# Kernel optimization log

Hardware: AMD Instinct MI355X
Metric: run time of the kernel (lower is better)

The kernel has to match this reference:

```python
import jax, jax.numpy as jnp
from jax import lax
import numpy as np

DIM, DT_RANK, D_INNER, D_STATE = 256, 16, 256, 16

def _ssm_params(key, d, dt_rank, d_inner, n):
    k1, k2, k3 = jax.random.split(key, 3)
    Wdbc = jax.random.normal(k1, (d, dt_rank + 2 * n), jnp.float32) * 0.02
    Wdt = jax.random.normal(k2, (dt_rank, d_inner), jnp.float32) * 0.02
    bdt = jax.random.normal(k3, (d_inner,), jnp.float32) * 0.02
    Alog = jnp.log(jnp.tile(jnp.arange(1, n + 1, dtype=jnp.float32), (d_inner, 1)))
    D = jnp.ones((d_inner,), jnp.float32)
    return Wdbc, Wdt, bdt, Alog, D

def setup_inputs() -> dict:
    key = jax.random.key(0)
    ks = jax.random.split(key, 10)
    x = jax.random.normal(ks[0], (4, 4096, DIM), jnp.float32)
    ln_g = jnp.ones((DIM,), jnp.float32)
    ln_b = jnp.zeros((DIM,), jnp.float32)
    Wp = jax.random.normal(ks[1], (DIM, DIM), jnp.float32) * 0.02
    bp = jnp.zeros((DIM,), jnp.float32)
    Wcf = jax.random.normal(ks[2], (DIM, DIM), jnp.float32) * 0.02  # conv1d k=1 == pointwise matmul
    bcf = jnp.zeros((DIM,), jnp.float32)
    Wcb = jax.random.normal(ks[3], (DIM, DIM), jnp.float32) * 0.02
    bcb = jnp.zeros((DIM,), jnp.float32)
    Wdbc_f, Wdt_f, bdt_f, Alog_f, D_f = _ssm_params(ks[4], DIM, DT_RANK, D_INNER, D_STATE)
    Wdbc_b, Wdt_b, bdt_b, Alog_b, D_b = _ssm_params(ks[5], DIM, DT_RANK, D_INNER, D_STATE)
    return dict(x=x, ln_g=ln_g, ln_b=ln_b, Wp=Wp, bp=bp, Wcf=Wcf, bcf=bcf, Wcb=Wcb, bcb=bcb,
                Wdbc_f=Wdbc_f, Wdt_f=Wdt_f, bdt_f=bdt_f, Alog_f=Alog_f, D_f=D_f,
                Wdbc_b=Wdbc_b, Wdt_b=Wdt_b, bdt_b=bdt_b, Alog_b=Alog_b, D_b=D_b)

def _layernorm(x, g, b, eps=1e-5):
    mu = jnp.mean(x, -1, keepdims=True)
    var = jnp.var(x, -1, keepdims=True)
    return (x - mu) * lax.rsqrt(var + eps) * g + b

def _selective_scan(x, delta, A, B, C, D):
    # x, delta: [b,s,d]; A: [d,n]; B, C: [b,s,n]; D: [d]
    deltaA = jnp.exp(delta[..., None] * A)              # [b,s,d,n]
    BX = delta[..., None] * B[:, :, None, :] * x[..., None]  # [b,s,d,n]
    dA = jnp.moveaxis(deltaA, 1, 0)
    bx = jnp.moveaxis(BX, 1, 0)
    def step(h, inp):
        dA_t, bx_t = inp
        h = dA_t * h + bx_t
        return h, h
    h0 = jnp.zeros_like(dA[0])
    _, hs = lax.scan(step, h0, (dA, bx))                # [s,b,d,n]
    hs = jnp.moveaxis(hs, 0, 1)                          # [b,s,d,n]
    y = jnp.einsum('bsdn,bsn->bsd', hs, C) + D * x
    return y

def _ssm(x, Wdbc, Wdt, bdt, Alog, D):
    A = -jnp.exp(Alog)
    dbc = x @ Wdbc
    dt_r, B, C = jnp.split(dbc, [DT_RANK, DT_RANK + D_STATE], axis=-1)
    delta = jax.nn.softplus(dt_r @ Wdt + bdt)
    return _selective_scan(x, delta, A, B, C, D)

def _process(x, Wc, bc, Wdbc, Wdt, bdt, Alog, D):
    x = jax.nn.softplus(x @ Wc.T + bc)  # Conv1d k=1: out[e] = sum_d W[e,d] x[d] + b[e]
    return _ssm(x, Wdbc, Wdt, bdt, Alog, D)

def reference(x, ln_g, ln_b, Wp, bp, Wcf, bcf, Wcb, bcb,
              Wdbc_f, Wdt_f, bdt_f, Alog_f, D_f,
              Wdbc_b, Wdt_b, bdt_b, Alog_b, D_b):
    skip = x
    xn = _layernorm(x, ln_g, ln_b)
    z1 = xn @ Wp + bp  # proj used for both z1 and x (same layer twice)
    xp = z1
    x1 = jax.nn.silu(_process(xp, Wcf, bcf, Wdbc_f, Wdt_f, bdt_f, Alog_f, D_f))
    x2r = _process(jnp.flip(xp, 1), Wcb, bcb, Wdbc_b, Wdt_b, bdt_b, Alog_b, D_b)
    x2 = jax.nn.silu(jnp.flip(x2r, 1))
    z = jax.nn.silu(z1)
    return x1 * z + x2 * z + skip
```

## Files before the change

kernel.cpp:

```cpp
#include <hip/hip_runtime.h>
#include <math.h>

#define SB 4
#define SS 4096
#define SD 256
#define SN 16
#define ROWS 16
#define NRB 1024
#define NCH 128
#define CHL 32

#define BM 128
#define BN 64
#define BK 64
#define LDT 72

#define MBM 32
#define MLDZ 264

typedef __attribute__((ext_vector_type(8))) short bf16x8;
typedef __attribute__((ext_vector_type(4))) float f32x4;

__device__ __forceinline__ unsigned short f2bf(float f){
    unsigned int u = __float_as_uint(f);
    u += 0x7FFFu + ((u >> 16) & 1u);
    return (unsigned short)(u >> 16);
}
__device__ __forceinline__ float bf2f(unsigned short u){
    return __uint_as_float(((unsigned int)u) << 16);
}
__device__ __forceinline__ float softplus_f(float x){
    return fmaxf(x, 0.f) + __logf(1.f + __expf(-fabsf(x)));
}
__device__ __forceinline__ float silu_f(float x){
    return x * __builtin_amdgcn_rcpf(1.f + __expf(-x));
}

__global__ __launch_bounds__(256)
void k_prep(const float* __restrict__ Wp,
            const float* __restrict__ Wcf, const float* __restrict__ Wcb,
            const float* __restrict__ Wdbc0, const float* __restrict__ Wdt0,
            const float* __restrict__ Wdbc1, const float* __restrict__ Wdt1,
            unsigned short* __restrict__ WpT, unsigned short* __restrict__ Wc,
            unsigned short* __restrict__ G3W)
{
    int idx = blockIdx.x*256 + threadIdx.x;
    if (idx < 65536){
        int n = idx >> 8, k = idx & 255;
        WpT[idx] = f2bf(Wp[k*256 + n]);
    } else if (idx < 65536 + 131072){
        int j = idx - 65536;
        Wc[j] = f2bf(j < 65536 ? Wcf[j] : Wcb[j - 65536]);
    } else {
        int j = idx - 196608;
        int dir = j / 81920; int r = j - dir*81920;
        int n = r >> 8, d = r & 255;
        const float* Wdbc = dir ? Wdbc1 : Wdbc0;
        const float* Wdt  = dir ? Wdt1  : Wdt0;
        float v;
        if (n < 256){
            v = 0.f;
            #pragma unroll
            for (int q = 0; q < 16; ++q)
                v = fmaf(Wdbc[d*48 + q], Wdt[q*256 + n], v);
        } else if (n < 272) v = Wdbc[d*48 + 16 + (n-256)];
        else if (n < 288)   v = Wdbc[d*48 + 32 + (n-272)];
        else                v = 0.f;
        G3W[(size_t)dir*81920 + r] = f2bf(v);
    }
}

__global__ __launch_bounds__(256)
void k_ln(const float* __restrict__ x, const float* __restrict__ g,
          const float* __restrict__ bln, unsigned short* __restrict__ xnbf){
    int row0 = blockIdx.x * ROWS;
    int tid = threadIdx.x; int w = tid >> 6; int lane = tid & 63;
    #pragma unroll
    for (int rep = 0; rep < 4; ++rep){
        int j = rep*4 + w;
        const float* xr = x + (size_t)(row0 + j)*SD;
        float4 v = *(const float4*)(xr + lane*4);
        float s = v.x + v.y + v.z + v.w;
        #pragma unroll
        for (int off = 32; off; off >>= 1) s += __shfl_xor(s, off, 64);
        float mu = s * (1.f/256.f);
        float d0 = v.x-mu, d1 = v.y-mu, d2 = v.z-mu, d3 = v.w-mu;
        float q = d0*d0 + d1*d1 + d2*d2 + d3*d3;
        #pragma unroll
        for (int off = 32; off; off >>= 1) q += __shfl_xor(q, off, 64);
        float rstd = rsqrtf(q*(1.f/256.f) + 1e-5f);
        float4 gg = *(const float4*)(g + lane*4);
        float4 bb = *(const float4*)(bln + lane*4);
        ushort4 o;
        o.x = f2bf(d0*rstd*gg.x + bb.x);
        o.y = f2bf(d1*rstd*gg.y + bb.y);
        o.z = f2bf(d2*rstd*gg.z + bb.z);
        o.w = f2bf(d3*rstd*gg.w + bb.w);
        *(ushort4*)(xnbf + (size_t)(row0+j)*SD + lane*4) = o;
    }
}

__global__ __launch_bounds__(256, 5)
void k_gemm0(const unsigned short* __restrict__ A,
             const unsigned short* __restrict__ Bt,
             const float* __restrict__ bias0,
             unsigned short* __restrict__ obf)
{
    __shared__ unsigned short sMem[(BM + BN) * LDT];
    unsigned short (*sA)[LDT] = (unsigned short (*)[LDT])sMem;
    unsigned short (*sB)[LDT] = (unsigned short (*)[LDT])(sMem + BM*LDT);
    int ntile = blockIdx.x, mtile = blockIdx.y;
    int row0 = mtile * BM;
    int col0 = ntile * BN;

    int tid = threadIdx.x;
    uint4 ra[4], rb[2];
    auto gload = [&](int kt){
        int k0 = kt * BK;
        #pragma unroll
        for (int i = 0; i < 4; ++i){
            int idx = tid + i*256; int r = idx >> 3, kp = idx & 7;
            ra[i] = *(const uint4*)(A + (size_t)(row0 + r)*256 + k0 + kp*8);
        }
        #pragma unroll
        for (int i = 0; i < 2; ++i){
            int idx = tid + i*256; int r = idx >> 3, kp = idx & 7;
            rb[i] = *(const uint4*)(Bt + (size_t)(col0 + r)*256 + k0 + kp*8);
        }
    };
    auto swrite = [&](){
        #pragma unroll
        for (int i = 0; i < 4; ++i){
            int idx = tid + i*256; int r = idx >> 3, kp = idx & 7;
            *(uint4*)&sA[r][kp*8] = ra[i];
        }
        #pragma unroll
        for (int i = 0; i < 2; ++i){
            int idx = tid + i*256; int r = idx >> 3, kp = idx & 7;
            *(uint4*)&sB[r][kp*8] = rb[i];
        }
    };

    gload(0); swrite(); __syncthreads();

    int lane = tid & 63, w = tid >> 6;
    int wr = w >> 1, wc = w & 1;
    int lr = lane & 15, hi = lane >> 4;

    f32x4 acc[4][2];
    #pragma unroll
    for (int mf = 0; mf < 4; ++mf)
        #pragma unroll
        for (int nf = 0; nf < 2; ++nf)
            acc[mf][nf] = f32x4{0.f, 0.f, 0.f, 0.f};

    for (int kt = 0; kt < 4; ++kt){
        if (kt < 3) gload(kt + 1);
        #pragma unroll
        for (int kk = 0; kk < BK; kk += 32){
            bf16x8 af[4], bfr[2];
            #pragma unroll
            for (int mf = 0; mf < 4; ++mf)
                af[mf] = *(const bf16x8*)&sA[wr*64 + mf*16 + lr][kk + hi*8];
            #pragma unroll
            for (int nf = 0; nf < 2; ++nf)
                bfr[nf] = *(const bf16x8*)&sB[wc*32 + nf*16 + lr][kk + hi*8];
            #pragma unroll
            for (int mf = 0; mf < 4; ++mf)
                #pragma unroll
                for (int nf = 0; nf < 2; ++nf)
                    acc[mf][nf] = __builtin_amdgcn_mfma_f32_16x16x32_bf16(
                        af[mf], bfr[nf], acc[mf][nf], 0, 0, 0);
        }
        if (kt < 3){
            __syncthreads();
            swrite();
            __syncthreads();
        }
    }

    __syncthreads();
    unsigned short (*sOut)[LDT] = (unsigned short (*)[LDT])sMem;
    #pragma unroll
    for (int mf = 0; mf < 4; ++mf){
        #pragma unroll
        for (int nf = 0; nf < 2; ++nf){
            int col = col0 + wc*32 + nf*16 + lr;
            float bias = bias0[col];
            #pragma unroll
            for (int r = 0; r < 4; ++r)
                sOut[wr*64 + mf*16 + hi*4 + r][wc*32 + nf*16 + lr] =
                    f2bf(acc[mf][nf][r] + bias);
        }
    }
    __syncthreads();
    #pragma unroll
    for (int p = 0; p < 4; ++p){
        int chunk = tid + p*256;
        int r = chunk >> 3, cg = chunk & 7;
        uint4 v = *(const uint4*)&sOut[r][cg*8];
        *(uint4*)(obf + (size_t)(row0 + r)*256 + col0 + cg*8) = v;
    }
}

__global__ __launch_bounds__(256, 4)
void k_mid(const unsigned short* __restrict__ z1bf,
           const unsigned short* __restrict__ Wc,
           const unsigned short* __restrict__ G3W,
           const float* __restrict__ bc0, const float* __restrict__ bc1,
           const float* __restrict__ bdt0, const float* __restrict__ bdt1,
           unsigned short* __restrict__ xcbf,
           unsigned short* __restrict__ dg0, unsigned short* __restrict__ dg1,
           float* __restrict__ Bg0, float* __restrict__ Bg1,
           float* __restrict__ Cg0, float* __restrict__ Cg1)
{
    __shared__ unsigned short sZ[MBM*MLDZ];
    __shared__ unsigned short sX[MBM*MLDZ];
    int mtile = blockIdx.x, dir = blockIdx.y;
    int row0 = mtile*MBM;
    int tid = threadIdx.x;
    int lane = tid & 63, w = tid >> 6;
    int lr = lane & 15, hi = lane >> 4;

    {
        const uint4* src = (const uint4*)(z1bf + (size_t)row0*256);
        #pragma unroll
        for (int p = 0; p < 4; ++p){
            int idx = tid + p*256;
            int r = idx >> 5, cq = idx & 31;
            *(uint4*)&sZ[r*MLDZ + cq*8] = src[idx];
        }
    }
    __syncthreads();

    const float* bcp  = dir ? bc1  : bc0;
    const float* bdtp = dir ? bdt1 : bdt0;
    unsigned short* dgp = dir ? dg1 : dg0;
    const unsigned short* Wcp = Wc + (size_t)dir*65536;
    const unsigned short* Gp  = G3W + (size_t)dir*81920;

    f32x4 acc1[4][2];
    #pragma unroll
    for (int nt1 = 0; nt1 < 4; ++nt1)
        #pragma unroll
        for (int mf = 0; mf < 2; ++mf)
            acc1[nt1][mf] = f32x4{0.f,0.f,0.f,0.f};
    #pragma unroll
    for (int kt = 0; kt < 4; ++kt){
        #pragma unroll
        for (int kk2 = 0; kk2 < 2; ++kk2){
            int ko = kt*64 + kk2*32 + hi*8;
            bf16x8 wf[4];
            #pragma unroll
            for (int nt1 = 0; nt1 < 4; ++nt1)
                wf[nt1] = *(const bf16x8*)(Wcp + (size_t)(nt1*64 + w*16 + lr)*256 + ko);
            bf16x8 zf0 = *(const bf16x8*)&sZ[(     lr)*MLDZ + ko];
            bf16x8 zf1 = *(const bf16x8*)&sZ[(16 + lr)*MLDZ + ko];
            #pragma unroll
            for (int nt1 = 0; nt1 < 4; ++nt1){
                acc1[nt1][0] = __builtin_amdgcn_mfma_f32_16x16x32_bf16(wf[nt1], zf0, acc1[nt1][0], 0,0,0);
                acc1[nt1][1] = __builtin_amdgcn_mfma_f32_16x16x32_bf16(wf[nt1], zf1, acc1[nt1][1], 0,0,0);
            }
        }
    }
    #pragma unroll
    for (int nt1 = 0; nt1 < 4; ++nt1){
        #pragma unroll
        for (int mf = 0; mf < 2; ++mf){
            float4 bb = *(const float4*)(bcp + nt1*64 + w*16 + hi*4);
            ushort4 o;
            o.x = f2bf(softplus_f(acc1[nt1][mf][0] + bb.x));
            o.y = f2bf(softplus_f(acc1[nt1][mf][1] + bb.y));
            o.z = f2bf(softplus_f(acc1[nt1][mf][2] + bb.z));
            o.w = f2bf(softplus_f(acc1[nt1][mf][3] + bb.w));
            *(ushort4*)&sX[(mf*16 + lr)*MLDZ + nt1*64 + w*16 + hi*4] = o;
        }
    }
    __syncthreads();
    {
        #pragma unroll
        for (int p = 0; p < 4; ++p){
            int idx = tid + p*256;
            int r = idx >> 5, cq = idx & 31;
            *(uint4*)(xcbf + (size_t)(row0 + r)*512 + dir*256 + cq*8) =
                *(const uint4*)&sX[r*MLDZ + cq*8];
        }
    }

    f32x4 acc2[5][2];
    #pragma unroll
    for (int t5 = 0; t5 < 5; ++t5)
        #pragma unroll
        for (int mf = 0; mf < 2; ++mf)
            acc2[t5][mf] = f32x4{0.f,0.f,0.f,0.f};
    #pragma unroll
    for (int nt1 = 0; nt1 < 4; ++nt1){
        bf16x8 af[2][2];
        #pragma unroll
        for (int mf = 0; mf < 2; ++mf)
            #pragma unroll
            for (int k2 = 0; k2 < 2; ++k2)
                af[mf][k2] = *(const bf16x8*)&sX[(mf*16 + lr)*MLDZ + nt1*64 + k2*32 + hi*8];
        #pragma unroll
        for (int k2 = 0; k2 < 2; ++k2){
            int ko = nt1*64 + k2*32 + hi*8;
            bf16x8 gf[5];
            #pragma unroll
            for (int nt2 = 0; nt2 < 5; ++nt2)
                gf[nt2] = *(const bf16x8*)(Gp + (size_t)(nt2*64 + w*16 + lr)*256 + ko);
            #pragma unroll
            for (int nt2 = 0; nt2 < 5; ++nt2){
                acc2[nt2][0] = __builtin_amdgcn_mfma_f32_16x16x32_bf16(gf[nt2], af[0][k2], acc2[nt2][0], 0,0,0);
                acc2[nt2][1] = __builtin_amdgcn_mfma_f32_16x16x32_bf16(gf[nt2], af[1][k2], acc2[nt2][1], 0,0,0);
            }
        }
    }

    #pragma unroll
    for (int nt2 = 0; nt2 < 4; ++nt2){
        #pragma unroll
        for (int mf = 0; mf < 2; ++mf){
            int tok = row0 + mf*16 + lr;
            int col = nt2*64 + w*16 + hi*4;
            float4 bb = *(const float4*)(bdtp + col);
            ushort4 o;
            o.x = f2bf(softplus_f(acc2[nt2][mf][0] + bb.x));
            o.y = f2bf(softplus_f(acc2[nt2][mf][1] + bb.y));
            o.z = f2bf(softplus_f(acc2[nt2][mf][2] + bb.z));
            o.w = f2bf(softplus_f(acc2[nt2][mf][3] + bb.w));
            *(ushort4*)(dgp + (size_t)tok*SD + col) = o;
        }
    }
    if (w < 2){
        float* P = (w == 0) ? (dir ? Bg1 : Bg0) : (dir ? Cg1 : Cg0);
        #pragma unroll
        for (int mf = 0; mf < 2; ++mf){
            int tok = row0 + mf*16 + lr;
            float4 v = { acc2[4][mf][0], acc2[4][mf][1], acc2[4][mf][2], acc2[4][mf][3] };
            *(float4*)(P + (size_t)tok*SN + hi*4) = v;
        }
    }
}

__global__ __launch_bounds__(256)
void k_scan_p1(const unsigned short* __restrict__ xcbf,
               const unsigned short* __restrict__ dg0, const float* __restrict__ B0, const float* __restrict__ Al0,
               const unsigned short* __restrict__ dg1, const float* __restrict__ B1, const float* __restrict__ Al1,
               float* __restrict__ hend, float* __restrict__ sdl)
{
    __shared__ float sB[CHL*SN];
    int blk = blockIdx.x;
    int c = blk & (NCH-1); int dir = (blk>>7) & 1; int b = blk>>8;
    const unsigned short* dg = dir ? dg1 : dg0;
    const float* Bg   = dir ? B1  : B0;
    const float* Alog = dir ? Al1 : Al0;
    const unsigned short* xc = xcbf + dir*256;
    int d = threadIdx.x;
    #pragma unroll
    for (int k = 0; k < 2; ++k){
        int li = threadIdx.x + k*256;
        int i = li >> 4, n = li & 15;
        int tau = c*CHL + i;
        int t = dir ? (SS-1-tau) : tau;
        sB[li] = Bg[((size_t)b*SS + t)*SN + n];
    }
    float A[SN];
    #pragma unroll
    for (int k = 0; k < 4; ++k){
        float4 al = *(const float4*)(Alog + d*SN + k*4);
        A[k*4+0] = -__expf(al.x); A[k*4+1] = -__expf(al.y);
        A[k*4+2] = -__expf(al.z); A[k*4+3] = -__expf(al.w);
    }
    __syncthreads();
    int t0 = dir ? (SS-1 - c*CHL) : (c*CHL);
    const unsigned short* pd = dg + ((size_t)b*SS + t0)*SD + d;
    const unsigned short* px = xc + ((size_t)b*SS + t0)*512 + d;
    int strided = dir ? -SD : SD;
    int stridex = dir ? -512 : 512;
    float h[SN];
    #pragma unroll
    for (int n = 0; n < SN; ++n) h[n] = 0.f;
    float sumdl = 0.f;
    float dl = bf2f(*pd), xv = bf2f(*px);
    for (int i = 0; i < CHL; ++i){
        float dlN = 0.f, xvN = 0.f;
        if (i+1 < CHL){ pd += strided; px += stridex; dlN = bf2f(*pd); xvN = bf2f(*px); }
        sumdl += dl;
        float dlx = dl * xv;
        const float4* b4 = (const float4*)&sB[i*SN];
        #pragma unroll
        for (int k = 0; k < 4; ++k){
            float4 bb = b4[k];
            h[k*4+0] = fmaf(__expf(dl*A[k*4+0]), h[k*4+0], bb.x*dlx);
            h[k*4+1] = fmaf(__expf(dl*A[k*4+1]), h[k*4+1], bb.y*dlx);
            h[k*4+2] = fmaf(__expf(dl*A[k*4+2]), h[k*4+2], bb.z*dlx);
            h[k*4+3] = fmaf(__expf(dl*A[k*4+3]), h[k*4+3], bb.w*dlx);
        }
        dl = dlN; xv = xvN;
    }
    size_t base = (((size_t)(b*2+dir)*NCH + c)*SD + d)*SN;
    #pragma unroll
    for (int k = 0; k < 4; ++k)
        *(float4*)(hend + base + k*4) = make_float4(h[k*4+0],h[k*4+1],h[k*4+2],h[k*4+3]);
    sdl[((size_t)(b*2+dir)*NCH + c)*SD + d] = sumdl;
}

__global__ __launch_bounds__(256)
void k_chain(const float* __restrict__ Al0, const float* __restrict__ Al1,
             float* hend, const float* __restrict__ sdl)
{
    int gidx = blockIdx.x*256 + threadIdx.x;
    int n = gidx & 15; int d = (gidx >> 4) & 255; int dirb = gidx >> 12;
    const float* Alog = (dirb & 1) ? Al1 : Al0;
    float A = -__expf(Alog[d*SN + n]);
    float H = 0.f;
    const size_t cs = (size_t)SD*SN;
    size_t idx  = (size_t)dirb*NCH*cs + (size_t)d*SN + n;
    size_t sidx = (size_t)dirb*NCH*SD + d;
    float he[4], sd[4];
    #pragma unroll
    for (int k = 0; k < 4; ++k){
        he[k] = hend[idx + (size_t)k*cs];
        sd[k] = sdl[sidx + (size_t)k*SD];
    }
    for (int cg = 0; cg < NCH; cg += 4){
        float heN[4] = {0.f,0.f,0.f,0.f};
        float sdN[4] = {0.f,0.f,0.f,0.f};
        if (cg + 4 < NCH){
            #pragma unroll
            for (int k = 0; k < 4; ++k){
                heN[k] = hend[idx + (size_t)(k+4)*cs];
                sdN[k] = sdl[sidx + (size_t)(k+4)*SD];
            }
        }
        #pragma unroll
        for (int k = 0; k < 4; ++k){
            hend[idx + (size_t)k*cs] = H;
            H = fmaf(__expf(A*sd[k]), H, he[k]);
        }
        #pragma unroll
        for (int k = 0; k < 4; ++k){ he[k] = heN[k]; sd[k] = sdN[k]; }
        idx += 4*cs; sidx += 4*SD;
    }
}

__global__ __launch_bounds__(256)
void k_scan_p2f(const unsigned short* __restrict__ xcbf,
                const unsigned short* __restrict__ dg0, const float* __restrict__ B0,
                const float* __restrict__ C0, const float* __restrict__ Al0,
                const float* __restrict__ Dv0,
                const unsigned short* __restrict__ dg1, const float* __restrict__ B1,
                const float* __restrict__ C1, const float* __restrict__ Al1,
                const float* __restrict__ Dv1,
                const float* __restrict__ hin,
                const unsigned short* __restrict__ z1bf,
                const float* __restrict__ x,
                float* __restrict__ out)
{
    __shared__ float yL[CHL*SD];
    __shared__ float sB0[CHL*SN], sC0[CHL*SN], sB1[CHL*SN], sC1[CHL*SN];
    int blk = blockIdx.x;
    int c = blk & (NCH-1); int b = blk >> 7;
    int d = threadIdx.x;
    #pragma unroll
    for (int k = 0; k < 2; ++k){
        int li = threadIdx.x + k*256;
        int i = li >> 4, n = li & 15;
        int tF = c*CHL + i;
        int tR = c*CHL + (CHL-1) - i;
        sB0[li] = B0[((size_t)b*SS + tF)*SN + n];
        sC0[li] = C0[((size_t)b*SS + tF)*SN + n];
        sB1[li] = B1[((size_t)b*SS + tR)*SN + n];
        sC1[li] = C1[((size_t)b*SS + tR)*SN + n];
    }
    __syncthreads();

    {
        float A[SN];
        #pragma unroll
        for (int k = 0; k < 4; ++k){
            float4 al = *(const float4*)(Al0 + d*SN + k*4);
            A[k*4+0] = -__expf(al.x); A[k*4+1] = -__expf(al.y);
            A[k*4+2] = -__expf(al.z); A[k*4+3] = -__expf(al.w);
        }
        float h[SN];
        size_t base = (((size_t)(b*2+0)*NCH + c)*SD + d)*SN;
        #pragma unroll
        for (int k = 0; k < 4; ++k){
            float4 hv = *(const float4*)(hin + base + k*4);
            h[k*4+0]=hv.x; h[k*4+1]=hv.y; h[k*4+2]=hv.z; h[k*4+3]=hv.w;
        }
        float Dd = Dv0[d];
        for (int i = 0; i < CHL; ++i){
            size_t rowb = (size_t)b*SS + c*CHL + i;
            float dl = bf2f(dg0[rowb*SD + d]);
            float xv = bf2f(xcbf[rowb*512 + d]);
            float dlx = dl * xv;
            float yv = Dd * xv;
            const float4* b4 = (const float4*)&sB0[i*SN];
            const float4* c4 = (const float4*)&sC0[i*SN];
            #pragma unroll
            for (int k = 0; k < 4; ++k){
                float4 bb = b4[k];
                float4 cc = c4[k];
                h[k*4+0] = fmaf(__expf(dl*A[k*4+0]), h[k*4+0], bb.x*dlx);
                yv = fmaf(h[k*4+0], cc.x, yv);
                h[k*4+1] = fmaf(__expf(dl*A[k*4+1]), h[k*4+1], bb.y*dlx);
                yv = fmaf(h[k*4+1], cc.y, yv);
                h[k*4+2] = fmaf(__expf(dl*A[k*4+2]), h[k*4+2], bb.z*dlx);
                yv = fmaf(h[k*4+2], cc.z, yv);
                h[k*4+3] = fmaf(__expf(dl*A[k*4+3]), h[k*4+3], bb.w*dlx);
                yv = fmaf(h[k*4+3], cc.w, yv);
            }
            yL[i*SD + d] = yv;
        }
    }
    {
        float A[SN];
        #pragma unroll
        for (int k = 0; k < 4; ++k){
            float4 al = *(const float4*)(Al1 + d*SN + k*4);
            A[k*4+0] = -__expf(al.x); A[k*4+1] = -__expf(al.y);
            A[k*4+2] = -__expf(al.z); A[k*4+3] = -__expf(al.w);
        }
        float h[SN];
        size_t base = (((size_t)(b*2+1)*NCH + (NCH-1-c))*SD + d)*SN;
        #pragma unroll
        for (int k = 0; k < 4; ++k){
            float4 hv = *(const float4*)(hin + base + k*4);
            h[k*4+0]=hv.x; h[k*4+1]=hv.y; h[k*4+2]=hv.z; h[k*4+3]=hv.w;
        }
        float Dd = Dv1[d];
        for (int ip = 0; ip < CHL; ++ip){
            int iloc = (CHL-1) - ip;
            size_t rowb = (size_t)b*SS + c*CHL + iloc;
            float dl = bf2f(dg1[rowb*SD + d]);
            float xv = bf2f(xcbf[rowb*512 + 256 + d]);
            float dlx = dl * xv;
            float yv = Dd * xv;
            const float4* b4 = (const float4*)&sB1[ip*SN];
            const float4* c4 = (const float4*)&sC1[ip*SN];
            #pragma unroll
            for (int k = 0; k < 4; ++k){
                float4 bb = b4[k];
                float4 cc = c4[k];
                h[k*4+0] = fmaf(__expf(dl*A[k*4+0]), h[k*4+0], bb.x*dlx);
                yv = fmaf(h[k*4+0], cc.x, yv);
                h[k*4+1] = fmaf(__expf(dl*A[k*4+1]), h[k*4+1], bb.y*dlx);
                yv = fmaf(h[k*4+1], cc.y, yv);
                h[k*4+2] = fmaf(__expf(dl*A[k*4+2]), h[k*4+2], bb.z*dlx);
                yv = fmaf(h[k*4+2], cc.z, yv);
                h[k*4+3] = fmaf(__expf(dl*A[k*4+3]), h[k*4+3], bb.w*dlx);
                yv = fmaf(h[k*4+3], cc.w, yv);
            }
            float y0v = yL[iloc*SD + d];
            float zv = bf2f(z1bf[rowb*SD + d]);
            float xo = x[rowb*SD + d];
            out[rowb*SD + d] = (silu_f(y0v) + silu_f(yv)) * silu_f(zv) + xo;
        }
    }
}

extern "C" void kernel_launch(void* const* d_in, const int* in_sizes, int n_in,
                              void* d_out, int out_size, void* d_ws, size_t ws_size,
                              hipStream_t stream) {
    const float* x     = (const float*)d_in[0];
    const float* ln_g  = (const float*)d_in[1];
    const float* ln_b  = (const float*)d_in[2];
    const float* Wp    = (const float*)d_in[3];
    const float* bp    = (const float*)d_in[4];
    const float* Wcf   = (const float*)d_in[5];
    const float* bcf   = (const float*)d_in[6];
    const float* Wcb   = (const float*)d_in[7];
    const float* bcb   = (const float*)d_in[8];
    const float* Wdbc_f= (const float*)d_in[9];
    const float* Wdt_f = (const float*)d_in[10];
    const float* bdt_f = (const float*)d_in[11];
    const float* Alog_f= (const float*)d_in[12];
    const float* D_f   = (const float*)d_in[13];
    const float* Wdbc_b= (const float*)d_in[14];
    const float* Wdt_b = (const float*)d_in[15];
    const float* bdt_b = (const float*)d_in[16];
    const float* Alog_b= (const float*)d_in[17];
    const float* D_b   = (const float*)d_in[18];
    float* out = (float*)d_out;

    float* ws = (float*)d_ws;
    const size_t NTOK  = (size_t)SB*SS;
    const size_t SZ_BD = NTOK*SD;
    const size_t SZ_BN = NTOK*SN;
    size_t off = 0;
    float* dgr   = ws + off; off += SZ_BD;
    unsigned short* dg0 = (unsigned short*)dgr;
    unsigned short* dg1 = dg0 + SZ_BD;
    float* Bg0   = ws + off; off += SZ_BN;
    float* Bg1   = ws + off; off += SZ_BN;
    float* Cg0   = ws + off; off += SZ_BN;
    float* Cg1   = ws + off; off += SZ_BN;
    float* regA  = ws + off; off += SZ_BD;
    unsigned short* xnbf = (unsigned short*)regA;
    unsigned short* z1bf = xnbf + SZ_BD;
    float* regB  = ws + off; off += SZ_BD;
    unsigned short* xcbf = (unsigned short*)regB;
    float* hend  = ws + off; off += SZ_BD;
    float* sdl   = ws + off; off += (size_t)8*NCH*SD;
    unsigned short* WpT  = (unsigned short*)(ws + off); off += 65536/2;
    unsigned short* Wc   = (unsigned short*)(ws + off); off += 131072/2;
    unsigned short* G3W  = (unsigned short*)(ws + off); off += 163840/2;

    k_prep<<<1408, 256, 0, stream>>>(Wp, Wcf, Wcb, Wdbc_f, Wdt_f, Wdbc_b, Wdt_b,
                                     WpT, Wc, G3W);
    k_ln<<<NRB, 256, 0, stream>>>(x, ln_g, ln_b, xnbf);
    k_gemm0<<<dim3(4,128), 256, 0, stream>>>(xnbf, WpT, bp, z1bf);
    k_mid<<<dim3(512,2), 256, 0, stream>>>(z1bf, Wc, G3W,
        bcf, bcb, bdt_f, bdt_b, xcbf,
        dg0, dg1, Bg0, Bg1, Cg0, Cg1);
    k_scan_p1<<<1024, 256, 0, stream>>>(xcbf, dg0, Bg0, Alog_f,
                                        dg1, Bg1, Alog_b, hend, sdl);
    k_chain<<<128, 256, 0, stream>>>(Alog_f, Alog_b, hend, sdl);
    k_scan_p2f<<<512, 256, 0, stream>>>(xcbf,
        dg0, Bg0, Cg0, Alog_f, D_f,
        dg1, Bg1, Cg1, Alog_b, D_b,
        hend, z1bf, x, out);
}
```

Before: 158.3 us.

## Register-prefetch weights and z1 in k_mid, drop sZ staging, rotate K order

The two GEMM loops in k_mid now load the next K-slice of weights (and z1 activations) into registers while issuing MFMAs on the current slice, a software double-buffer. The z1 tile is no longer staged through shared memory; fragments are read directly from global, which removes one LDS buffer and a barrier and lowers LDS use per block. The K iteration order is rotated by mtile so that concurrent blocks read different weight columns, spreading cache and channel traffic. This raises register pressure, which could hurt occupancy under the 256x4 launch bound.

```diff
diff --git a/kernel.cpp b/kernel.cpp
--- a/kernel.cpp
+++ b/kernel.cpp
@@ -214,30 +214,21 @@
            float* __restrict__ Bg0, float* __restrict__ Bg1,
            float* __restrict__ Cg0, float* __restrict__ Cg1)
 {
-    __shared__ unsigned short sZ[MBM*MLDZ];
     __shared__ unsigned short sX[MBM*MLDZ];
     int mtile = blockIdx.x, dir = blockIdx.y;
     int row0 = mtile*MBM;
     int tid = threadIdx.x;
     int lane = tid & 63, w = tid >> 6;
     int lr = lane & 15, hi = lane >> 4;
-
-    {
-        const uint4* src = (const uint4*)(z1bf + (size_t)row0*256);
-        #pragma unroll
-        for (int p = 0; p < 4; ++p){
-            int idx = tid + p*256;
-            int r = idx >> 5, cq = idx & 31;
-            *(uint4*)&sZ[r*MLDZ + cq*8] = src[idx];
-        }
-    }
-    __syncthreads();
+    int rot = mtile & 3;
 
     const float* bcp  = dir ? bc1  : bc0;
     const float* bdtp = dir ? bdt1 : bdt0;
     unsigned short* dgp = dir ? dg1 : dg0;
     const unsigned short* Wcp = Wc + (size_t)dir*65536;
     const unsigned short* Gp  = G3W + (size_t)dir*81920;
+    const unsigned short* z0p = z1bf + (size_t)(row0 +      lr)*256;
+    const unsigned short* z1p = z1bf + (size_t)(row0 + 16 + lr)*256;
 
     f32x4 acc1[4][2];
     #pragma unroll
@@ -245,22 +236,38 @@
         #pragma unroll
         for (int mf = 0; mf < 2; ++mf)
             acc1[nt1][mf] = f32x4{0.f,0.f,0.f,0.f};
-    #pragma unroll
-    for (int kt = 0; kt < 4; ++kt){
-        #pragma unroll
-        for (int kk2 = 0; kk2 < 2; ++kk2){
-            int ko = kt*64 + kk2*32 + hi*8;
-            bf16x8 wf[4];
+
+    bf16x8 wf[4], zf0, zf1;
+    {
+        int ko = rot*64 + hi*8;
+        #pragma unroll
+        for (int nt1 = 0; nt1 < 4; ++nt1)
+            wf[nt1] = *(const bf16x8*)(Wcp + (size_t)(nt1*64 + w*16 + lr)*256 + ko);
+        zf0 = *(const bf16x8*)(z0p + ko);
+        zf1 = *(const bf16x8*)(z1p + ko);
+    }
+    #pragma unroll
+    for (int it = 0; it < 8; ++it){
+        bf16x8 wfn[4], zf0n, zf1n;
+        if (it < 7){
+            int itn = it + 1;
+            int kt = (((itn >> 1) + rot) & 3);
+            int ko = kt*64 + (itn & 1)*32 + hi*8;
             #pragma unroll
             for (int nt1 = 0; nt1 < 4; ++nt1)
-                wf[nt1] = *(const bf16x8*)(Wcp + (size_t)(nt1*64 + w*16 + lr)*256 + ko);
-            bf16x8 zf0 = *(const bf16x8*)&sZ[(     lr)*MLDZ + ko];
-            bf16x8 zf1 = *(const bf16x8*)&sZ[(16 + lr)*MLDZ + ko];
-            #pragma unroll
-            for (int nt1 = 0; nt1 < 4; ++nt1){
-                acc1[nt1][0] = __builtin_amdgcn_mfma_f32_16x16x32_bf16(wf[nt1], zf0, acc1[nt1][0], 0,0,0);
-                acc1[nt1][1] = __builtin_amdgcn_mfma_f32_16x16x32_bf16(wf[nt1], zf1, acc1[nt1][1], 0,0,0);
-            }
+                wfn[nt1] = *(const bf16x8*)(Wcp + (size_t)(nt1*64 + w*16 + lr)*256 + ko);
+            zf0n = *(const bf16x8*)(z0p + ko);
+            zf1n = *(const bf16x8*)(z1p + ko);
+        }
+        #pragma unroll
+        for (int nt1 = 0; nt1 < 4; ++nt1){
+            acc1[nt1][0] = __builtin_amdgcn_mfma_f32_16x16x32_bf16(wf[nt1], zf0, acc1[nt1][0], 0,0,0);
+            acc1[nt1][1] = __builtin_amdgcn_mfma_f32_16x16x32_bf16(wf[nt1], zf1, acc1[nt1][1], 0,0,0);
+        }
+        if (it < 7){
+            #pragma unroll
+            for (int nt1 = 0; nt1 < 4; ++nt1) wf[nt1] = wfn[nt1];
+            zf0 = zf0n; zf1 = zf1n;
         }
     }
     #pragma unroll
@@ -293,26 +300,37 @@
         #pragma unroll
         for (int mf = 0; mf < 2; ++mf)
             acc2[t5][mf] = f32x4{0.f,0.f,0.f,0.f};
-    #pragma unroll
-    for (int nt1 = 0; nt1 < 4; ++nt1){
-        bf16x8 af[2][2];
-        #pragma unroll
-        for (int mf = 0; mf < 2; ++mf)
-            #pragma unroll
-            for (int k2 = 0; k2 < 2; ++k2)
-                af[mf][k2] = *(const bf16x8*)&sX[(mf*16 + lr)*MLDZ + nt1*64 + k2*32 + hi*8];
-        #pragma unroll
-        for (int k2 = 0; k2 < 2; ++k2){
-            int ko = nt1*64 + k2*32 + hi*8;
-            bf16x8 gf[5];
+
+    bf16x8 gf[5];
+    {
+        int ko = rot*64 + hi*8;
+        #pragma unroll
+        for (int nt2 = 0; nt2 < 5; ++nt2)
+            gf[nt2] = *(const bf16x8*)(Gp + (size_t)(nt2*64 + w*16 + lr)*256 + ko);
+    }
+    #pragma unroll
+    for (int it = 0; it < 8; ++it){
+        int nt1 = (((it >> 1) + rot) & 3);
+        int ko  = nt1*64 + (it & 1)*32 + hi*8;
+        bf16x8 a0 = *(const bf16x8*)&sX[(     lr)*MLDZ + ko];
+        bf16x8 a1 = *(const bf16x8*)&sX[(16 + lr)*MLDZ + ko];
+        bf16x8 gfn[5];
+        if (it < 7){
+            int itn = it + 1;
+            int nt1n = (((itn >> 1) + rot) & 3);
+            int kon  = nt1n*64 + (itn & 1)*32 + hi*8;
             #pragma unroll
             for (int nt2 = 0; nt2 < 5; ++nt2)
-                gf[nt2] = *(const bf16x8*)(Gp + (size_t)(nt2*64 + w*16 + lr)*256 + ko);
-            #pragma unroll
-            for (int nt2 = 0; nt2 < 5; ++nt2){
-                acc2[nt2][0] = __builtin_amdgcn_mfma_f32_16x16x32_bf16(gf[nt2], af[0][k2], acc2[nt2][0], 0,0,0);
-                acc2[nt2][1] = __builtin_amdgcn_mfma_f32_16x16x32_bf16(gf[nt2], af[1][k2], acc2[nt2][1], 0,0,0);
-            }
+                gfn[nt2] = *(const bf16x8*)(Gp + (size_t)(nt2*64 + w*16 + lr)*256 + kon);
+        }
+        #pragma unroll
+        for (int nt2 = 0; nt2 < 5; ++nt2){
+            acc2[nt2][0] = __builtin_amdgcn_mfma_f32_16x16x32_bf16(gf[nt2], a0, acc2[nt2][0], 0,0,0);
+            acc2[nt2][1] = __builtin_amdgcn_mfma_f32_16x16x32_bf16(gf[nt2], a1, acc2[nt2][1], 0,0,0);
+        }
+        if (it < 7){
+            #pragma unroll
+            for (int nt2 = 0; nt2 < 5; ++nt2) gf[nt2] = gfn[nt2];
         }
     }
 
```

Measured after the change: 163.1 us. +3.0%, slower.

## Split fused mid kernel into two LDS-tiled double-buffered GEMM kernels

Applied to the files above, without the earlier changes.

Replaces the fused k_mid kernel, which streamed weight fragments straight from global memory for each 32-row tile, with two separate tiled GEMM kernels. The first computes the conv-projection plus softplus for both directions as one 512-wide output. The second computes the delta/B/C projection, with register-prefetched 128x64 tiles staged through LDS. This raises weight reuse per block and MFMA density. In exchange it adds a kernel launch and a global round trip of the intermediate activations between the two GEMMs.

```diff
diff --git a/kernel.cpp b/kernel.cpp
--- a/kernel.cpp
+++ b/kernel.cpp
@@ -14,9 +14,6 @@
 #define BN 64
 #define BK 64
 #define LDT 72
-
-#define MBM 32
-#define MLDZ 264
 
 typedef __attribute__((ext_vector_type(8))) short bf16x8;
 typedef __attribute__((ext_vector_type(4))) float f32x4;
@@ -203,141 +200,239 @@
     }
 }
 
-__global__ __launch_bounds__(256, 4)
-void k_mid(const unsigned short* __restrict__ z1bf,
-           const unsigned short* __restrict__ Wc,
-           const unsigned short* __restrict__ G3W,
-           const float* __restrict__ bc0, const float* __restrict__ bc1,
-           const float* __restrict__ bdt0, const float* __restrict__ bdt1,
-           unsigned short* __restrict__ xcbf,
-           unsigned short* __restrict__ dg0, unsigned short* __restrict__ dg1,
-           float* __restrict__ Bg0, float* __restrict__ Bg1,
-           float* __restrict__ Cg0, float* __restrict__ Cg1)
+__global__ __launch_bounds__(256, 5)
+void k_gemm1(const unsigned short* __restrict__ A,
+             const unsigned short* __restrict__ Bt,
+             const float* __restrict__ bc0, const float* __restrict__ bc1,
+             unsigned short* __restrict__ obf)
 {
-    __shared__ unsigned short sZ[MBM*MLDZ];
-    __shared__ unsigned short sX[MBM*MLDZ];
-    int mtile = blockIdx.x, dir = blockIdx.y;
-    int row0 = mtile*MBM;
+    __shared__ unsigned short sMem[(BM + BN) * LDT];
+    unsigned short (*sA)[LDT] = (unsigned short (*)[LDT])sMem;
+    unsigned short (*sB)[LDT] = (unsigned short (*)[LDT])(sMem + BM*LDT);
+    int ntile = blockIdx.x, mtile = blockIdx.y;
+    int row0 = mtile * BM;
+    int col0 = ntile * BN;
+
     int tid = threadIdx.x;
+    uint4 ra[4], rb[2];
+    auto gload = [&](int kt){
+        int k0 = kt * BK;
+        #pragma unroll
+        for (int i = 0; i < 4; ++i){
+            int idx = tid + i*256; int r = idx >> 3, kp = idx & 7;
+            ra[i] = *(const uint4*)(A + (size_t)(row0 + r)*256 + k0 + kp*8);
+        }
+        #pragma unroll
+        for (int i = 0; i < 2; ++i){
+            int idx = tid + i*256; int r = idx >> 3, kp = idx & 7;
+            rb[i] = *(const uint4*)(Bt + (size_t)(col0 + r)*256 + k0 + kp*8);
+        }
+    };
+    auto swrite = [&](){
+        #pragma unroll
+        for (int i = 0; i < 4; ++i){
+            int idx = tid + i*256; int r = idx >> 3, kp = idx & 7;
+            *(uint4*)&sA[r][kp*8] = ra[i];
+        }
+        #pragma unroll
+        for (int i = 0; i < 2; ++i){
+            int idx = tid + i*256; int r = idx >> 3, kp = idx & 7;
+            *(uint4*)&sB[r][kp*8] = rb[i];
+        }
+    };
+
+    gload(0); swrite(); __syncthreads();
+
     int lane = tid & 63, w = tid >> 6;
+    int wr = w >> 1, wc = w & 1;
     int lr = lane & 15, hi = lane >> 4;
 
-    {
-        const uint4* src = (const uint4*)(z1bf + (size_t)row0*256);
+    f32x4 acc[4][2];
+    #pragma unroll
+    for (int mf = 0; mf < 4; ++mf)
+        #pragma unroll
+        for (int nf = 0; nf < 2; ++nf)
+            acc[mf][nf] = f32x4{0.f, 0.f, 0.f, 0.f};
+
+    for (int kt = 0; kt < 4; ++kt){
+        if (kt < 3) gload(kt + 1);
+        #pragma unroll
+        for (int kk = 0; kk < BK; kk += 32){
+            bf16x8 af[4], bfr[2];
+            #pragma unroll
+            for (int mf = 0; mf < 4; ++mf)
+                af[mf] = *(const bf16x8*)&sA[wr*64 + mf*16 + lr][kk + hi*8];
+            #pragma unroll
+            for (int nf = 0; nf < 2; ++nf)
+                bfr[nf] = *(const bf16x8*)&sB[wc*32 + nf*16 + lr][kk + hi*8];
+            #pragma unroll
+            for (int mf = 0; mf < 4; ++mf)
+                #pragma unroll
+                for (int nf = 0; nf < 2; ++nf)
+                    acc[mf][nf] = __builtin_amdgcn_mfma_f32_16x16x32_bf16(
+                        af[mf], bfr[nf], acc[mf][nf], 0, 0, 0);
+        }
+        if (kt < 3){
+            __syncthreads();
+            swrite();
+            __syncthreads();
+        }
+    }
+
+    __syncthreads();
+    unsigned short (*sOut)[LDT] = (unsigned short (*)[LDT])sMem;
+    #pragma unroll
+    for (int mf = 0; mf < 4; ++mf){
+        #pragma unroll
+        for (int nf = 0; nf < 2; ++nf){
+            int col = col0 + wc*32 + nf*16 + lr;
+            float bias = (col < 256) ? bc0[col] : bc1[col - 256];
+            #pragma unroll
+            for (int r = 0; r < 4; ++r)
+                sOut[wr*64 + mf*16 + hi*4 + r][wc*32 + nf*16 + lr] =
+                    f2bf(softplus_f(acc[mf][nf][r] + bias));
+        }
+    }
+    __syncthreads();
+    #pragma unroll
+    for (int p = 0; p < 4; ++p){
+        int chunk = tid + p*256;
+        int r = chunk >> 3, cg = chunk & 7;
+        uint4 v = *(const uint4*)&sOut[r][cg*8];
+        *(uint4*)(obf + (size_t)(row0 + r)*512 + col0 + cg*8) = v;
+    }
+}
+
+__global__ __launch_bounds__(256, 5)
+void k_gemm2(const unsigned short* __restrict__ Abase,
+             const unsigned short* __restrict__ G3W,
+             const float* __restrict__ bdt0, const float* __restrict__ bdt1,
+             unsigned short* __restrict__ dg0, unsigned short* __restrict__ dg1,
+             float* __restrict__ Bg0, float* __restrict__ Bg1,
+             float* __restrict__ Cg0, float* __restrict__ Cg1)
+{
+    __shared__ unsigned short sMem[(BM + BN) * LDT];
+    unsigned short (*sA)[LDT] = (unsigned short (*)[LDT])sMem;
+    unsigned short (*sB)[LDT] = (unsigned short (*)[LDT])(sMem + BM*LDT);
+    int ntile = blockIdx.x, mtile = blockIdx.y;
+    int dir = blockIdx.z;
+    int row0 = mtile * BM;
+    int col0 = ntile * BN;
+    const unsigned short* A   = Abase + dir*256;
+    const unsigned short* Btp = G3W + (size_t)dir*81920;
+
+    int tid = threadIdx.x;
+    uint4 ra[4], rb[2];
+    auto gload = [&](int kt){
+        int k0 = kt * BK;
+        #pragma unroll
+        for (int i = 0; i < 4; ++i){
+            int idx = tid + i*256; int r = idx >> 3, kp = idx & 7;
+            ra[i] = *(const uint4*)(A + (size_t)(row0 + r)*512 + k0 + kp*8);
+        }
+        #pragma unroll
+        for (int i = 0; i < 2; ++i){
+            int idx = tid + i*256; int r = idx >> 3, kp = idx & 7;
+            rb[i] = *(const uint4*)(Btp + (size_t)(col0 + r)*256 + k0 + kp*8);
+        }
+    };
+    auto swrite = [&](){
+        #pragma unroll
+        for (int i = 0; i < 4; ++i){
+            int idx = tid + i*256; int r = idx >> 3, kp = idx & 7;
+            *(uint4*)&sA[r][kp*8] = ra[i];
+        }
+        #pragma unroll
+        for (int i = 0; i < 2; ++i){
+            int idx = tid + i*256; int r = idx >> 3, kp = idx & 7;
+            *(uint4*)&sB[r][kp*8] = rb[i];
+        }
+    };
+
+    gload(0); swrite(); __syncthreads();
+
+    int lane = tid & 63, w = tid >> 6;
+    int wr = w >> 1, wc = w & 1;
+    int lr = lane & 15, hi = lane >> 4;
+
+    f32x4 acc[4][2];
+    #pragma unroll
+    for (int mf = 0; mf < 4; ++mf)
+        #pragma unroll
+        for (int nf = 0; nf < 2; ++nf)
+            acc[mf][nf] = f32x4{0.f, 0.f, 0.f, 0.f};
+
+    for (int kt = 0; kt < 4; ++kt){
+        if (kt < 3) gload(kt + 1);
+        #pragma unroll
+        for (int kk = 0; kk < BK; kk += 32){
+            bf16x8 af[4], bfr[2];
+            #pragma unroll
+            for (int mf = 0; mf < 4; ++mf)
+                af[mf] = *(const bf16x8*)&sA[wr*64 + mf*16 + lr][kk + hi*8];
+            #pragma unroll
+            for (int nf = 0; nf < 2; ++nf)
+                bfr[nf] = *(const bf16x8*)&sB[wc*32 + nf*16 + lr][kk + hi*8];
+            #pragma unroll
+            for (int mf = 0; mf < 4; ++mf)
+                #pragma unroll
+                for (int nf = 0; nf < 2; ++nf)
+                    acc[mf][nf] = __builtin_amdgcn_mfma_f32_16x16x32_bf16(
+                        af[mf], bfr[nf], acc[mf][nf], 0, 0, 0);
+        }
+        if (kt < 3){
+            __syncthreads();
+            swrite();
+            __syncthreads();
+        }
+    }
+
+    __syncthreads();
+    if (ntile < 4){
+        const float* bdtp = dir ? bdt1 : bdt0;
+        unsigned short* dgp = dir ? dg1 : dg0;
+        unsigned short (*sOut)[LDT] = (unsigned short (*)[LDT])sMem;
+        #pragma unroll
+        for (int mf = 0; mf < 4; ++mf){
+            #pragma unroll
+            for (int nf = 0; nf < 2; ++nf){
+                int col = col0 + wc*32 + nf*16 + lr;
+                float bias = bdtp[col];
+                #pragma unroll
+                for (int r = 0; r < 4; ++r)
+                    sOut[wr*64 + mf*16 + hi*4 + r][wc*32 + nf*16 + lr] =
+                        f2bf(softplus_f(acc[mf][nf][r] + bias));
+            }
+        }
+        __syncthreads();
         #pragma unroll
         for (int p = 0; p < 4; ++p){
-            int idx = tid + p*256;
-            int r = idx >> 5, cq = idx & 31;
-            *(uint4*)&sZ[r*MLDZ + cq*8] = src[idx];
-        }
-    }
-    __syncthreads();
-
-    const float* bcp  = dir ? bc1  : bc0;
-    const float* bdtp = dir ? bdt1 : bdt0;
-    unsigned short* dgp = dir ? dg1 : dg0;
-    const unsigned short* Wcp = Wc + (size_t)dir*65536;
-    const unsigned short* Gp  = G3W + (size_t)dir*81920;
-
-    f32x4 acc1[4][2];
-    #pragma unroll
-    for (int nt1 = 0; nt1 < 4; ++nt1)
-        #pragma unroll
-        for (int mf = 0; mf < 2; ++mf)
-            acc1[nt1][mf] = f32x4{0.f,0.f,0.f,0.f};
-    #pragma unroll
-    for (int kt = 0; kt < 4; ++kt){
-        #pragma unroll
-        for (int kk2 = 0; kk2 < 2; ++kk2){
-            int ko = kt*64 + kk2*32 + hi*8;
-            bf16x8 wf[4];
-            #pragma unroll
-            for (int nt1 = 0; nt1 < 4; ++nt1)
-                wf[nt1] = *(const bf16x8*)(Wcp + (size_t)(nt1*64 + w*16 + lr)*256 + ko);
-            bf16x8 zf0 = *(const bf16x8*)&sZ[(     lr)*MLDZ + ko];
-            bf16x8 zf1 = *(const bf16x8*)&sZ[(16 + lr)*MLDZ + ko];
-            #pragma unroll
-            for (int nt1 = 0; nt1 < 4; ++nt1){
-                acc1[nt1][0] = __builtin_amdgcn_mfma_f32_16x16x32_bf16(wf[nt1], zf0, acc1[nt1][0], 0,0,0);
-                acc1[nt1][1] = __builtin_amdgcn_mfma_f32_16x16x32_bf16(wf[nt1], zf1, acc1[nt1][1], 0,0,0);
-            }
-        }
-    }
-    #pragma unroll
-    for (int nt1 = 0; nt1 < 4; ++nt1){
-        #pragma unroll
-        for (int mf = 0; mf < 2; ++mf){
-            float4 bb = *(const float4*)(bcp + nt1*64 + w*16 + hi*4);
-            ushort4 o;
-            o.x = f2bf(softplus_f(acc1[nt1][mf][0] + bb.x));
-            o.y = f2bf(softplus_f(acc1[nt1][mf][1] + bb.y));
-            o.z = f2bf(softplus_f(acc1[nt1][mf][2] + bb.z));
-            o.w = f2bf(softplus_f(acc1[nt1][mf][3] + bb.w));
-            *(ushort4*)&sX[(mf*16 + lr)*MLDZ + nt1*64 + w*16 + hi*4] = o;
-        }
-    }
-    __syncthreads();
-    {
-        #pragma unroll
-        for (int p = 0; p < 4; ++p){
-            int idx = tid + p*256;
-            int r = idx >> 5, cq = idx & 31;
-            *(uint4*)(xcbf + (size_t)(row0 + r)*512 + dir*256 + cq*8) =
-                *(const uint4*)&sX[r*MLDZ + cq*8];
-        }
-    }
-
-    f32x4 acc2[5][2];
-    #pragma unroll
-    for (int t5 = 0; t5 < 5; ++t5)
-        #pragma unroll
-        for (int mf = 0; mf < 2; ++mf)
-            acc2[t5][mf] = f32x4{0.f,0.f,0.f,0.f};
-    #pragma unroll
-    for (int nt1 = 0; nt1 < 4; ++nt1){
-        bf16x8 af[2][2];
-        #pragma unroll
-        for (int mf = 0; mf < 2; ++mf)
-            #pragma unroll
-            for (int k2 = 0; k2 < 2; ++k2)
-                af[mf][k2] = *(const bf16x8*)&sX[(mf*16 + lr)*MLDZ + nt1*64 + k2*32 + hi*8];
-        #pragma unroll
-        for (int k2 = 0; k2 < 2; ++k2){
-            int ko = nt1*64 + k2*32 + hi*8;
-            bf16x8 gf[5];
-            #pragma unroll
-            for (int nt2 = 0; nt2 < 5; ++nt2)
-                gf[nt2] = *(const bf16x8*)(Gp + (size_t)(nt2*64 + w*16 + lr)*256 + ko);
-            #pragma unroll
-            for (int nt2 = 0; nt2 < 5; ++nt2){
-                acc2[nt2][0] = __builtin_amdgcn_mfma_f32_16x16x32_bf16(gf[nt2], af[0][k2], acc2[nt2][0], 0,0,0);
-                acc2[nt2][1] = __builtin_amdgcn_mfma_f32_16x16x32_bf16(gf[nt2], af[1][k2], acc2[nt2][1], 0,0,0);
-            }
-        }
-    }
-
-    #pragma unroll
-    for (int nt2 = 0; nt2 < 4; ++nt2){
-        #pragma unroll
-        for (int mf = 0; mf < 2; ++mf){
-            int tok = row0 + mf*16 + lr;
-            int col = nt2*64 + w*16 + hi*4;
-            float4 bb = *(const float4*)(bdtp + col);
-            ushort4 o;
-            o.x = f2bf(softplus_f(acc2[nt2][mf][0] + bb.x));
-            o.y = f2bf(softplus_f(acc2[nt2][mf][1] + bb.y));
-            o.z = f2bf(softplus_f(acc2[nt2][mf][2] + bb.z));
-            o.w = f2bf(softplus_f(acc2[nt2][mf][3] + bb.w));
-            *(ushort4*)(dgp + (size_t)tok*SD + col) = o;
-        }
-    }
-    if (w < 2){
-        float* P = (w == 0) ? (dir ? Bg1 : Bg0) : (dir ? Cg1 : Cg0);
-        #pragma unroll
-        for (int mf = 0; mf < 2; ++mf){
-            int tok = row0 + mf*16 + lr;
-            float4 v = { acc2[4][mf][0], acc2[4][mf][1], acc2[4][mf][2], acc2[4][mf][3] };
-            *(float4*)(P + (size_t)tok*SN + hi*4) = v;
+            int chunk = tid + p*256;
+            int r = chunk >> 3, cg = chunk & 7;
+            uint4 v = *(const uint4*)&sOut[r][cg*8];
+            *(uint4*)(dgp + (size_t)(row0 + r)*256 + col0 + cg*8) = v;
+        }
+    } else {
+        float* sEF = (float*)sMem;
+        if (wc == 0){
+            #pragma unroll
+            for (int mf = 0; mf < 4; ++mf)
+                #pragma unroll
+                for (int nf = 0; nf < 2; ++nf)
+                    #pragma unroll
+                    for (int r = 0; r < 4; ++r)
+                        sEF[(wr*64 + mf*16 + hi*4 + r)*36 + nf*16 + lr] =
+                            acc[mf][nf][r];
+        }
+        __syncthreads();
+        float* Bp = dir ? Bg1 : Bg0;
+        float* Cp = dir ? Cg1 : Cg0;
+        #pragma unroll
+        for (int p = 0; p < 2; ++p){
+            int chunk = tid + p*256;
+            int r = chunk >> 2, q = chunk & 3;
+            *(float4*)(Bp + (size_t)(row0 + r)*SN + q*4) = *(const float4*)&sEF[r*36 + q*4];
+            *(float4*)(Cp + (size_t)(row0 + r)*SN + q*4) = *(const float4*)&sEF[r*36 + 16 + q*4];
         }
     }
 }
@@ -612,8 +707,8 @@
                                      WpT, Wc, G3W);
     k_ln<<<NRB, 256, 0, stream>>>(x, ln_g, ln_b, xnbf);
     k_gemm0<<<dim3(4,128), 256, 0, stream>>>(xnbf, WpT, bp, z1bf);
-    k_mid<<<dim3(512,2), 256, 0, stream>>>(z1bf, Wc, G3W,
-        bcf, bcb, bdt_f, bdt_b, xcbf,
+    k_gemm1<<<dim3(8,128), 256, 0, stream>>>(z1bf, Wc, bcf, bcb, xcbf);
+    k_gemm2<<<dim3(5,128,2), 256, 0, stream>>>(xcbf, G3W, bdt_f, bdt_b,
         dg0, dg1, Bg0, Bg1, Cg0, Cg1);
     k_scan_p1<<<1024, 256, 0, stream>>>(xcbf, dg0, Bg0, Alog_f,
                                         dg1, Bg1, Alog_b, hend, sdl);
```

After: 198.7 us. +25.5%, slower.

## Fuse chunk-local scan pass into k_mid using shared-memory delta, x and B

Applied to the files above, without the earlier changes.

Removes the separate k_scan_p1 kernel and computes each chunk's local end state and delta sum inside k_mid. The mid kernel already holds the 32-token tile of x in shared memory, and now also stages delta and B there. This avoids one launch and the global re-read of delta, x and B. The cost is a serial 32-step scan added at the end of k_mid, which may stretch the GEMM kernel and lower its overlap. Backward-direction chunk indices are remapped so the results match the old layout.

```diff
diff --git a/kernel.cpp b/kernel.cpp
--- a/kernel.cpp
+++ b/kernel.cpp
@@ -209,13 +209,17 @@
            const unsigned short* __restrict__ G3W,
            const float* __restrict__ bc0, const float* __restrict__ bc1,
            const float* __restrict__ bdt0, const float* __restrict__ bdt1,
+           const float* __restrict__ Al0, const float* __restrict__ Al1,
            unsigned short* __restrict__ xcbf,
            unsigned short* __restrict__ dg0, unsigned short* __restrict__ dg1,
            float* __restrict__ Bg0, float* __restrict__ Bg1,
-           float* __restrict__ Cg0, float* __restrict__ Cg1)
+           float* __restrict__ Cg0, float* __restrict__ Cg1,
+           float* __restrict__ hend, float* __restrict__ sdl)
 {
     __shared__ unsigned short sZ[MBM*MLDZ];
     __shared__ unsigned short sX[MBM*MLDZ];
+    __shared__ float sBn[MBM*SN];
+    unsigned short* sDG = sZ;
     int mtile = blockIdx.x, dir = blockIdx.y;
     int row0 = mtile*MBM;
     int tid = threadIdx.x;
@@ -235,6 +239,7 @@
 
     const float* bcp  = dir ? bc1  : bc0;
     const float* bdtp = dir ? bdt1 : bdt0;
+    const float* Alp  = dir ? Al1  : Al0;
     unsigned short* dgp = dir ? dg1 : dg0;
     const unsigned short* Wcp = Wc + (size_t)dir*65536;
     const unsigned short* Gp  = G3W + (size_t)dir*81920;
@@ -320,7 +325,7 @@
     for (int nt2 = 0; nt2 < 4; ++nt2){
         #pragma unroll
         for (int mf = 0; mf < 2; ++mf){
-            int tok = row0 + mf*16 + lr;
+            int tokl = mf*16 + lr;
             int col = nt2*64 + w*16 + hi*4;
             float4 bb = *(const float4*)(bdtp + col);
             ushort4 o;
@@ -328,81 +333,60 @@
             o.y = f2bf(softplus_f(acc2[nt2][mf][1] + bb.y));
             o.z = f2bf(softplus_f(acc2[nt2][mf][2] + bb.z));
             o.w = f2bf(softplus_f(acc2[nt2][mf][3] + bb.w));
-            *(ushort4*)(dgp + (size_t)tok*SD + col) = o;
+            *(ushort4*)(dgp + (size_t)(row0 + tokl)*SD + col) = o;
+            *(ushort4*)&sDG[tokl*MLDZ + col] = o;
         }
     }
     if (w < 2){
         float* P = (w == 0) ? (dir ? Bg1 : Bg0) : (dir ? Cg1 : Cg0);
         #pragma unroll
         for (int mf = 0; mf < 2; ++mf){
-            int tok = row0 + mf*16 + lr;
+            int tokl = mf*16 + lr;
             float4 v = { acc2[4][mf][0], acc2[4][mf][1], acc2[4][mf][2], acc2[4][mf][3] };
-            *(float4*)(P + (size_t)tok*SN + hi*4) = v;
-        }
-    }
-}
-
-__global__ __launch_bounds__(256)
-void k_scan_p1(const unsigned short* __restrict__ xcbf,
-               const unsigned short* __restrict__ dg0, const float* __restrict__ B0, const float* __restrict__ Al0,
-               const unsigned short* __restrict__ dg1, const float* __restrict__ B1, const float* __restrict__ Al1,
-               float* __restrict__ hend, float* __restrict__ sdl)
-{
-    __shared__ float sB[CHL*SN];
-    int blk = blockIdx.x;
-    int c = blk & (NCH-1); int dir = (blk>>7) & 1; int b = blk>>8;
-    const unsigned short* dg = dir ? dg1 : dg0;
-    const float* Bg   = dir ? B1  : B0;
-    const float* Alog = dir ? Al1 : Al0;
-    const unsigned short* xc = xcbf + dir*256;
-    int d = threadIdx.x;
-    #pragma unroll
-    for (int k = 0; k < 2; ++k){
-        int li = threadIdx.x + k*256;
-        int i = li >> 4, n = li & 15;
-        int tau = c*CHL + i;
-        int t = dir ? (SS-1-tau) : tau;
-        sB[li] = Bg[((size_t)b*SS + t)*SN + n];
-    }
-    float A[SN];
-    #pragma unroll
-    for (int k = 0; k < 4; ++k){
-        float4 al = *(const float4*)(Alog + d*SN + k*4);
-        A[k*4+0] = -__expf(al.x); A[k*4+1] = -__expf(al.y);
-        A[k*4+2] = -__expf(al.z); A[k*4+3] = -__expf(al.w);
+            *(float4*)(P + (size_t)(row0 + tokl)*SN + hi*4) = v;
+            if (w == 0) *(float4*)&sBn[tokl*SN + hi*4] = v;
+        }
     }
     __syncthreads();
-    int t0 = dir ? (SS-1 - c*CHL) : (c*CHL);
-    const unsigned short* pd = dg + ((size_t)b*SS + t0)*SD + d;
-    const unsigned short* px = xc + ((size_t)b*SS + t0)*512 + d;
-    int strided = dir ? -SD : SD;
-    int stridex = dir ? -512 : 512;
-    float h[SN];
-    #pragma unroll
-    for (int n = 0; n < SN; ++n) h[n] = 0.f;
-    float sumdl = 0.f;
-    float dl = bf2f(*pd), xv = bf2f(*px);
-    for (int i = 0; i < CHL; ++i){
-        float dlN = 0.f, xvN = 0.f;
-        if (i+1 < CHL){ pd += strided; px += stridex; dlN = bf2f(*pd); xvN = bf2f(*px); }
-        sumdl += dl;
-        float dlx = dl * xv;
-        const float4* b4 = (const float4*)&sB[i*SN];
+
+    {
+        int d = tid;
+        float A[SN];
         #pragma unroll
         for (int k = 0; k < 4; ++k){
-            float4 bb = b4[k];
-            h[k*4+0] = fmaf(__expf(dl*A[k*4+0]), h[k*4+0], bb.x*dlx);
-            h[k*4+1] = fmaf(__expf(dl*A[k*4+1]), h[k*4+1], bb.y*dlx);
-            h[k*4+2] = fmaf(__expf(dl*A[k*4+2]), h[k*4+2], bb.z*dlx);
-            h[k*4+3] = fmaf(__expf(dl*A[k*4+3]), h[k*4+3], bb.w*dlx);
-        }
-        dl = dlN; xv = xvN;
-    }
-    size_t base = (((size_t)(b*2+dir)*NCH + c)*SD + d)*SN;
-    #pragma unroll
-    for (int k = 0; k < 4; ++k)
-        *(float4*)(hend + base + k*4) = make_float4(h[k*4+0],h[k*4+1],h[k*4+2],h[k*4+3]);
-    sdl[((size_t)(b*2+dir)*NCH + c)*SD + d] = sumdl;
+            float4 al = *(const float4*)(Alp + d*SN + k*4);
+            A[k*4+0] = -__expf(al.x); A[k*4+1] = -__expf(al.y);
+            A[k*4+2] = -__expf(al.z); A[k*4+3] = -__expf(al.w);
+        }
+        float h[SN];
+        #pragma unroll
+        for (int n = 0; n < SN; ++n) h[n] = 0.f;
+        float sumdl = 0.f;
+        for (int i = 0; i < CHL; ++i){
+            int tl = dir ? (CHL-1-i) : i;
+            float dl = bf2f(sDG[tl*MLDZ + d]);
+            float xv = bf2f(sX[tl*MLDZ + d]);
+            sumdl += dl;
+            float dlx = dl * xv;
+            const float4* b4 = (const float4*)&sBn[tl*SN];
+            #pragma unroll
+            for (int k = 0; k < 4; ++k){
+                float4 bb = b4[k];
+                h[k*4+0] = fmaf(__expf(dl*A[k*4+0]), h[k*4+0], bb.x*dlx);
+                h[k*4+1] = fmaf(__expf(dl*A[k*4+1]), h[k*4+1], bb.y*dlx);
+                h[k*4+2] = fmaf(__expf(dl*A[k*4+2]), h[k*4+2], bb.z*dlx);
+                h[k*4+3] = fmaf(__expf(dl*A[k*4+3]), h[k*4+3], bb.w*dlx);
+            }
+        }
+        int b = mtile >> 7, s = mtile & 127;
+        int ceff = dir ? (NCH-1 - s) : s;
+        size_t cbase = ((size_t)(b*2+dir)*NCH + ceff)*SD + d;
+        size_t base = cbase*SN;
+        #pragma unroll
+        for (int k = 0; k < 4; ++k)
+            *(float4*)(hend + base + k*4) = make_float4(h[k*4+0],h[k*4+1],h[k*4+2],h[k*4+3]);
+        sdl[cbase] = sumdl;
+    }
 }
 
 __global__ __launch_bounds__(256)
@@ -613,10 +597,8 @@
     k_ln<<<NRB, 256, 0, stream>>>(x, ln_g, ln_b, xnbf);
     k_gemm0<<<dim3(4,128), 256, 0, stream>>>(xnbf, WpT, bp, z1bf);
     k_mid<<<dim3(512,2), 256, 0, stream>>>(z1bf, Wc, G3W,
-        bcf, bcb, bdt_f, bdt_b, xcbf,
-        dg0, dg1, Bg0, Bg1, Cg0, Cg1);
-    k_scan_p1<<<1024, 256, 0, stream>>>(xcbf, dg0, Bg0, Alog_f,
-                                        dg1, Bg1, Alog_b, hend, sdl);
+        bcf, bcb, bdt_f, bdt_b, Alog_f, Alog_b, xcbf,
+        dg0, dg1, Bg0, Bg1, Cg0, Cg1, hend, sdl);
     k_chain<<<128, 256, 0, stream>>>(Alog_f, Alog_b, hend, sdl);
     k_scan_p2f<<<512, 256, 0, stream>>>(xcbf,
         dg0, Bg0, Cg0, Alog_f, D_f,
```

After: 147.6 us. -6.8%, faster.
